# Kernel tuning notes

Hardware: AMD Instinct MI355X
Metric: run time of the kernel (lower is better)

The kernel has to match this reference:

```python
import jax, jax.numpy as jnp
import numpy as np

MAX_SEGMENTS = 196
MAX_PIX = 400        # max_pixels_per_segment
C = 3                # n_channels
EMBED = 768


def setup_inputs() -> dict:
    key = jax.random.key(0)
    k1, k2, k3, k4 = jax.random.split(key, 4)
    B, H, W = 64, 224, 224
    img = jax.random.normal(k1, (B, C, H, W), jnp.float32)
    segments = jax.random.randint(k2, (B, H, W), 0, MAX_SEGMENTS).astype(jnp.int32)
    fan_in = C * MAX_PIX
    Wp = jax.random.normal(k3, (EMBED, fan_in), jnp.float32) / np.sqrt(fan_in)
    b = jax.random.normal(k4, (EMBED,), jnp.float32) * 0.01
    return {"img": img, "segments": segments, "W": Wp, "b": b}


def _gather_pad(img_flat, seg_flat):
    # img_flat: [C, P], seg_flat: [P] int32. Builds [S, C*MAX_PIX] padded buffer.
    P = seg_flat.shape[0]
    order = jnp.argsort(seg_flat, stable=True)          # stable -> keeps scan order (matches torch truncation)
    s = seg_flat[order]                                  # sorted segment ids, [P]
    counts = jnp.zeros((MAX_SEGMENTS,), jnp.int32).at[seg_flat].add(1)
    starts = jnp.concatenate([jnp.zeros((1,), jnp.int32),
                              jnp.cumsum(counts)[:-1].astype(jnp.int32)])
    rank = jnp.arange(P, dtype=jnp.int32) - starts[s]    # within-segment position
    valid = rank < MAX_PIX                               # truncate overly large segments
    rank_c = jnp.where(valid, rank, 0)
    vals = jnp.where(valid[:, None], img_flat.T[order], 0.0)  # [P, C]
    buf = jnp.zeros((MAX_SEGMENTS, C, MAX_PIX), img_flat.dtype)
    buf = buf.at[s, :, rank_c].add(vals)                 # invalid rows add zeros -> no-op
    # torch does pixels_in_segment.flatten() on (C, MAX_PIX) -> channel-major layout
    return buf.reshape(MAX_SEGMENTS, C * MAX_PIX)


def reference(img, segments, W, b):
    B = img.shape[0]
    img_flat = img.reshape(B, C, -1)          # [B, C, H*W]
    seg_flat = segments.reshape(B, -1)        # [B, H*W]
    feats = jax.vmap(_gather_pad)(img_flat, seg_flat)   # [B, S, C*MAX_PIX]
    return jnp.einsum('bsf,ef->bse', feats, W) + b      # nn.Linear
```

## Files before the change

kernel.cpp:

```cpp
#include <hip/hip_runtime.h>
#include <hip/hip_bf16.h>

#define B_      64
#define C_      3
#define H_      224
#define W_      224
#define P_      (H_*W_)
#define S_      196
#define MAXPIX  400
#define E_      768
#define K_      1200
#define KP_     1216
#define CHUNK_  512
#define NCH_    (P_/CHUNK_)
#define M_      (B_*S_)
#define QPR_    304
#define GQ_GRID 4096

typedef __attribute__((ext_vector_type(8))) short short8;
typedef __attribute__((ext_vector_type(4))) float f32x4;

__device__ inline unsigned short f2bf(float f) {
  union { float f; unsigned int u; } x; x.f = f;
  return (unsigned short)((x.u + 0x7fffu + ((x.u >> 16) & 1u)) >> 16);
}

__device__ inline int xcd_chunk(int wg, int nwg) {
  int q = nwg >> 3;
  return (wg & 7) * q + (wg >> 3);
}

__global__ void wconv_k(const float* __restrict__ Wf, unsigned short* __restrict__ Wb) {
  int idx = blockIdx.x * 256 + threadIdx.x;
  int e = idx / KP_, k = idx - e * KP_;
  float v = (k < K_) ? Wf[e * K_ + k] : 0.f;
  Wb[idx] = f2bf(v);
}

__global__ __launch_bounds__(512) void rank_k(const int* __restrict__ seg,
                                              int* __restrict__ hist,
                                              unsigned short* __restrict__ rloc) {
  int b = blockIdx.x / NCH_, ch = blockIdx.x % NCH_;
  int tid = threadIdx.x, wave = tid >> 6, lane = tid & 63;
  int p = ch * CHUNK_ + tid;
  int s = seg[b * P_ + p];

  __shared__ int lhist[8][S_];
  for (int i = tid; i < 8 * S_; i += 512) ((int*)lhist)[i] = 0;
  __syncthreads();

  int r = 0;
  #pragma unroll 1
  for (int j = 0; j < 64; ++j) {
    int sj = __shfl(s, j);
    r += (j < lane && sj == s) ? 1 : 0;
  }
  atomicAdd(&lhist[wave][s], 1);
  __syncthreads();

  int off = 0;
  for (int w2 = 0; w2 < wave; ++w2) off += lhist[w2][s];
  rloc[b * P_ + p] = (unsigned short)(off + r);

  if (tid < S_) {
    int t = 0;
    #pragma unroll
    for (int w2 = 0; w2 < 8; ++w2) t += lhist[w2][tid];
    hist[(b * NCH_ + ch) * S_ + tid] = t;
  }
}

__global__ __launch_bounds__(128) void prefix_k(int* __restrict__ hist, int* __restrict__ cnts) {
  int b = blockIdx.x / S_, s = blockIdx.x % S_;
  int t = threadIdx.x;
  __shared__ int sc[128];
  int v = (t < NCH_) ? hist[(b * NCH_ + t) * S_ + s] : 0;
  sc[t] = v;
  __syncthreads();
  #pragma unroll
  for (int off = 1; off < 128; off <<= 1) {
    int x = (t >= off) ? sc[t - off] : 0;
    __syncthreads();
    sc[t] += x;
    __syncthreads();
  }
  if (t < NCH_) hist[(b * NCH_ + t) * S_ + s] = sc[t] - v;
  if (t == NCH_ - 1) {
    int tot = sc[t];
    cnts[b * S_ + s] = tot < MAXPIX ? tot : MAXPIX;
  }
}

__global__ __launch_bounds__(256) void scatter_inv_k(const int* __restrict__ seg,
                                                     const int* __restrict__ starts,
                                                     const unsigned short* __restrict__ rloc,
                                                     unsigned short* __restrict__ inv) {
  int wg = xcd_chunk(blockIdx.x, B_ * (P_ / 256));
  int b = wg / (P_ / 256);
  int p = (wg % (P_ / 256)) * 256 + threadIdx.x;
  int s = seg[b * P_ + p];
  int rank = starts[(b * NCH_ + (p >> 9)) * S_ + s] + rloc[b * P_ + p];
  if (rank < MAXPIX)
    inv[(b * S_ + s) * MAXPIX + rank] = (unsigned short)p;
}

__global__ __launch_bounds__(256) void gather_k(const float* __restrict__ img,
                                                const unsigned short* __restrict__ inv,
                                                const int* __restrict__ cnts,
                                                unsigned short* __restrict__ feats) {
  const int nq = M_ * QPR_;
  int blk = xcd_chunk(blockIdx.x, GQ_GRID);
  for (int q = blk * 256 + threadIdx.x; q < nq; q += GQ_GRID * 256) {
    int row = q / QPR_;
    int qi = q - row * QPR_;
    unsigned short* frow = feats + (size_t)row * KP_;
    if (qi >= 300) {
      *(ushort4*)&frow[K_ + ((qi - 300) << 2)] = make_ushort4(0, 0, 0, 0);
      continue;
    }
    int c = qi / 100;
    int r4 = (qi - c * 100) << 2;
    int b = row / S_;
    int cnt = cnts[row];
    ushort4 pq = *(const ushort4*)&inv[(size_t)row * MAXPIX + r4];
    const float* ic = img + ((size_t)b * C_ + c) * P_;
    ushort4 o;
    o.x = (r4 + 0 < cnt) ? f2bf(ic[pq.x]) : (unsigned short)0;
    o.y = (r4 + 1 < cnt) ? f2bf(ic[pq.y]) : (unsigned short)0;
    o.z = (r4 + 2 < cnt) ? f2bf(ic[pq.z]) : (unsigned short)0;
    o.w = (r4 + 3 < cnt) ? f2bf(ic[pq.w]) : (unsigned short)0;
    *(ushort4*)&frow[c * MAXPIX + r4] = o;
  }
}

__global__ __launch_bounds__(256) void gemm_k(const unsigned short* __restrict__ A,
                                              const unsigned short* __restrict__ Bw,
                                              const float* __restrict__ bias,
                                              float* __restrict__ out) {
  int bid;
  {
    int wg = blockIdx.x, q = 588 / 8, r = 588 % 8;
    int xcd = wg % 8, idx = wg / 8;
    bid = (xcd < r) ? xcd * (q + 1) + idx : r * (q + 1) + (xcd - r) * q + idx;
  }
  const int nb = bid % (E_ / 128);
  const int mb = bid / (E_ / 128);
  const int tid = threadIdx.x;
  const int w = tid >> 6, l = tid & 63;
  const int wr = w >> 1, wc = w & 1;

  __shared__ __align__(16) unsigned short As[128 * 32];
  __shared__ __align__(16) unsigned short Bs[128 * 32];

  f32x4 acc[4][4] = {};

  const int lrow = l >> 2;
  const int lcol = (l & 3) * 8;
  const int kk = (l >> 4) * 8;

  for (int k0 = 0; k0 < KP_; k0 += 32) {
    #pragma unroll
    for (int q = 0; q < 2; ++q) {
      int r = (w * 2 + q) * 16 + lrow;
      const unsigned short* ga = A + (size_t)(mb * 128 + r) * KP_ + k0 + lcol;
      __builtin_amdgcn_global_load_lds((const __attribute__((address_space(1))) unsigned int*)ga,
                                       (__attribute__((address_space(3))) unsigned int*)&As[(w * 2 + q) * 512],
                                       16, 0, 0);
      const unsigned short* gb = Bw + (size_t)(nb * 128 + r) * KP_ + k0 + lcol;
      __builtin_amdgcn_global_load_lds((const __attribute__((address_space(1))) unsigned int*)gb,
                                       (__attribute__((address_space(3))) unsigned int*)&Bs[(w * 2 + q) * 512],
                                       16, 0, 0);
    }
    __syncthreads();

    short8 af[4], bf[4];
    #pragma unroll
    for (int mi = 0; mi < 4; ++mi)
      af[mi] = *(const short8*)&As[(wr * 64 + mi * 16 + (l & 15)) * 32 + kk];
    #pragma unroll
    for (int ni = 0; ni < 4; ++ni)
      bf[ni] = *(const short8*)&Bs[(wc * 64 + ni * 16 + (l & 15)) * 32 + kk];
    #pragma unroll
    for (int mi = 0; mi < 4; ++mi)
      #pragma unroll
      for (int ni = 0; ni < 4; ++ni)
        acc[mi][ni] = __builtin_amdgcn_mfma_f32_16x16x32_bf16(af[mi], bf[ni], acc[mi][ni], 0, 0, 0);
    __syncthreads();
  }

  const int r0 = (l >> 4) * 4;
  const int c0 = l & 15;
  #pragma unroll
  for (int mi = 0; mi < 4; ++mi) {
    #pragma unroll
    for (int ni = 0; ni < 4; ++ni) {
      int col = nb * 128 + wc * 64 + ni * 16 + c0;
      float bv = bias[col];
      int row = mb * 128 + wr * 64 + mi * 16 + r0;
      #pragma unroll
      for (int r = 0; r < 4; ++r)
        out[(size_t)(row + r) * E_ + col] = acc[mi][ni][r] + bv;
    }
  }
}

extern "C" void kernel_launch(void* const* d_in, const int* in_sizes, int n_in,
                              void* d_out, int out_size, void* d_ws, size_t ws_size,
                              hipStream_t stream) {
  const float* img  = (const float*)d_in[0];
  const int*   seg  = (const int*)d_in[1];
  const float* Wf   = (const float*)d_in[2];
  const float* bias = (const float*)d_in[3];
  float* out = (float*)d_out;

  constexpr size_t WB_BYTES    = (size_t)E_ * KP_ * 2;
  constexpr size_t INV_BYTES   = (size_t)M_ * MAXPIX * 2;
  constexpr size_t CNT_BYTES   = (size_t)M_ * 4;
  constexpr size_t RLOC_BYTES  = (size_t)B_ * P_ * 2;
  char* ws = (char*)d_ws;
  unsigned short* Wb    = (unsigned short*)ws;
  unsigned short* inv   = (unsigned short*)(ws + WB_BYTES);
  int*            cnts  = (int*)(ws + WB_BYTES + INV_BYTES);
  unsigned short* feats = (unsigned short*)(ws + WB_BYTES + INV_BYTES + CNT_BYTES);
  unsigned short* rloc  = feats;
  int*            hist  = (int*)((char*)feats + RLOC_BYTES);

  wconv_k<<<(E_ * KP_) / 256, 256, 0, stream>>>(Wf, Wb);
  rank_k<<<B_ * NCH_, 512, 0, stream>>>(seg, hist, rloc);
  prefix_k<<<B_ * S_, 128, 0, stream>>>(hist, cnts);
  scatter_inv_k<<<B_ * (P_ / 256), 256, 0, stream>>>(seg, hist, rloc, inv);
  gather_k<<<GQ_GRID, 256, 0, stream>>>(img, inv, cnts, feats);
  gemm_k<<<(M_ / 128) * (E_ / 128), 256, 0, stream>>>(feats, Wb, bias, out);
}
```

Measured before the change: 260.1 us.

## Pack image into pixel-major bf16 layout and permute weight K order

Adds a pre-pass that converts the image to bf16 and packs the three channels of each pixel into one 8-byte ushort4. The gather kernel can then fetch all channels of a pixel with a single random load instead of three scattered fp32 loads. The weight conversion permutes the K dimension to pixel-major order to match the new feature layout. The output buffer serves as scratch space for the packed image, and the extra pass adds one more full read and write of the image.

```diff
diff --git a/kernel.cpp b/kernel.cpp
--- a/kernel.cpp
+++ b/kernel.cpp
@@ -14,8 +14,9 @@
 #define CHUNK_  512
 #define NCH_    (P_/CHUNK_)
 #define M_      (B_*S_)
-#define QPR_    304
+#define QPR2    104
 #define GQ_GRID 4096
+
 
 typedef __attribute__((ext_vector_type(8))) short short8;
 typedef __attribute__((ext_vector_type(4))) float f32x4;
@@ -30,10 +31,27 @@
   return (wg & 7) * q + (wg >> 3);
 }
 
+__global__ __launch_bounds__(256) void imgt_k(const float* __restrict__ img,
+                                              ushort4* __restrict__ imgT) {
+  int i = blockIdx.x * 256 + threadIdx.x;
+  int b = i / P_, p = i - b * P_;
+  const float* ib = img + (size_t)b * C_ * P_;
+  ushort4 o;
+  o.x = f2bf(ib[p]);
+  o.y = f2bf(ib[P_ + p]);
+  o.z = f2bf(ib[2 * P_ + p]);
+  o.w = 0;
+  imgT[i] = o;
+}
+
 __global__ void wconv_k(const float* __restrict__ Wf, unsigned short* __restrict__ Wb) {
   int idx = blockIdx.x * 256 + threadIdx.x;
   int e = idx / KP_, k = idx - e * KP_;
-  float v = (k < K_) ? Wf[e * K_ + k] : 0.f;
+  float v = 0.f;
+  if (k < K_) {
+    int r = k / 3, c = k - r * 3;
+    v = Wf[e * K_ + c * MAXPIX + r];
+  }
   Wb[idx] = f2bf(v);
 }
 
@@ -104,32 +122,34 @@
     inv[(b * S_ + s) * MAXPIX + rank] = (unsigned short)p;
 }
 
-__global__ __launch_bounds__(256) void gather_k(const float* __restrict__ img,
+__global__ __launch_bounds__(256) void gather_k(const ushort4* __restrict__ imgT,
                                                 const unsigned short* __restrict__ inv,
                                                 const int* __restrict__ cnts,
                                                 unsigned short* __restrict__ feats) {
-  const int nq = M_ * QPR_;
+  const int nq = M_ * QPR2;
   int blk = xcd_chunk(blockIdx.x, GQ_GRID);
   for (int q = blk * 256 + threadIdx.x; q < nq; q += GQ_GRID * 256) {
-    int row = q / QPR_;
-    int qi = q - row * QPR_;
+    int row = q / QPR2;
+    int qi = q - row * QPR2;
     unsigned short* frow = feats + (size_t)row * KP_;
-    if (qi >= 300) {
-      *(ushort4*)&frow[K_ + ((qi - 300) << 2)] = make_ushort4(0, 0, 0, 0);
+    if (qi >= 100) {
+      *(ushort4*)&frow[K_ + ((qi - 100) << 2)] = make_ushort4(0, 0, 0, 0);
       continue;
     }
-    int c = qi / 100;
-    int r4 = (qi - c * 100) << 2;
+    int r4 = qi << 2;
+    int cnt = cnts[row];
     int b = row / S_;
-    int cnt = cnts[row];
     ushort4 pq = *(const ushort4*)&inv[(size_t)row * MAXPIX + r4];
-    const float* ic = img + ((size_t)b * C_ + c) * P_;
-    ushort4 o;
-    o.x = (r4 + 0 < cnt) ? f2bf(ic[pq.x]) : (unsigned short)0;
-    o.y = (r4 + 1 < cnt) ? f2bf(ic[pq.y]) : (unsigned short)0;
-    o.z = (r4 + 2 < cnt) ? f2bf(ic[pq.z]) : (unsigned short)0;
-    o.w = (r4 + 3 < cnt) ? f2bf(ic[pq.w]) : (unsigned short)0;
-    *(ushort4*)&frow[c * MAXPIX + r4] = o;
+    const ushort4* it = imgT + (size_t)b * P_;
+    ushort4 z = make_ushort4(0, 0, 0, 0);
+    ushort4 v0 = (r4 + 0 < cnt) ? it[pq.x] : z;
+    ushort4 v1 = (r4 + 1 < cnt) ? it[pq.y] : z;
+    ushort4 v2 = (r4 + 2 < cnt) ? it[pq.z] : z;
+    ushort4 v3 = (r4 + 3 < cnt) ? it[pq.w] : z;
+    ushort4* dst = (ushort4*)&frow[r4 * 3];
+    dst[0] = make_ushort4(v0.x, v0.y, v0.z, v1.x);
+    dst[1] = make_ushort4(v1.y, v1.z, v2.x, v2.y);
+    dst[2] = make_ushort4(v2.z, v3.x, v3.y, v3.z);
   }
 }
 
@@ -224,11 +244,13 @@
   unsigned short* feats = (unsigned short*)(ws + WB_BYTES + INV_BYTES + CNT_BYTES);
   unsigned short* rloc  = feats;
   int*            hist  = (int*)((char*)feats + RLOC_BYTES);
-
+  ushort4*        imgT  = (ushort4*)d_out;
+
+  imgt_k<<<(B_ * P_) / 256, 256, 0, stream>>>(img, imgT);
   wconv_k<<<(E_ * KP_) / 256, 256, 0, stream>>>(Wf, Wb);
   rank_k<<<B_ * NCH_, 512, 0, stream>>>(seg, hist, rloc);
   prefix_k<<<B_ * S_, 128, 0, stream>>>(hist, cnts);
   scatter_inv_k<<<B_ * (P_ / 256), 256, 0, stream>>>(seg, hist, rloc, inv);
-  gather_k<<<GQ_GRID, 256, 0, stream>>>(img, inv, cnts, feats);
+  gather_k<<<GQ_GRID, 256, 0, stream>>>(imgT, inv, cnts, feats);
   gemm_k<<<(M_ / 128) * (E_ / 128), 256, 0, stream>>>(feats, Wb, bias, out);
 }
```

Result: slower. 269.1 us (+3.5%).
